# Optimization experiments

Measured on AMD Instinct MI355X. Metric: run time of the kernel, lower is better.

Reference implementation:

```python
import jax, jax.numpy as jnp
import numpy as np

NEG = -1e9


def _siglu(x):
    return x * jax.nn.sigmoid(x)


def setup_inputs() -> dict:
    key = jax.random.key(0)
    ks = jax.random.split(key, 10)
    B, S, M, D = 2, 2048, 64, 1024
    sc = 0.02
    return {
        "tokens": jax.random.normal(ks[0], (B, S, D), jnp.float32),
        "memory": jax.random.normal(ks[1], (B, M, D), jnp.float32),
        "Wq": jax.random.normal(ks[2], (D, D), jnp.float32) * sc,
        "bq": jnp.zeros((D,), jnp.float32),
        "Wk": jax.random.normal(ks[3], (D, D), jnp.float32) * sc,
        "bk": jnp.zeros((D,), jnp.float32),
        "Wv": jax.random.normal(ks[4], (D, D), jnp.float32) * sc,
        "bv": jnp.zeros((D,), jnp.float32),
        "Wo": jax.random.normal(ks[5], (D, D), jnp.float32) * sc,
        "bo": jnp.zeros((D,), jnp.float32),
        "pool_q": jax.random.normal(ks[6], (M, D), jnp.float32),
        "cell_W": jax.random.normal(ks[7], (2 * D, 2 * D), jnp.float32) * sc,
        "cell_b": jnp.zeros((2 * D,), jnp.float32),
    }


def reference(tokens, memory, Wq, bq, Wk, bk, Wv, bv, Wo, bo, pool_q, cell_W, cell_b):
    B, S, D = tokens.shape
    M = memory.shape[1]
    H = 16
    hd = D // H
    T = M + S

    x = jnp.concatenate([memory, tokens], axis=1)  # (B, T, D)

    # combined causal mask: memory rows/cols fully visible, token block causal
    tok_mask = jnp.triu(jnp.full((S, S), NEG, jnp.float32), k=1)
    mask = jnp.zeros((T, T), jnp.float32).at[M:, M:].set(tok_mask)  # (T, T)

    def heads(w, b):
        return (x @ w.T + b).reshape(B, T, H, hd).transpose(0, 2, 1, 3)

    q = heads(Wq, bq)  # (B, H, T, hd)
    k = heads(Wk, bk)
    v = heads(Wv, bv)

    scores = jnp.einsum("bhqd,bhkd->bhqk", q, k) * (hd ** -0.5) + mask
    attn = jax.nn.softmax(scores, axis=-1)
    ctx = jnp.einsum("bhqk,bhkd->bhqd", attn, v)
    ctx = ctx.transpose(0, 2, 1, 3).reshape(B, T, D)
    attn_out = ctx @ Wo.T + bo

    x = x + attn_out  # residual
    mem_out = x[:, :M]  # (B, M, D)
    tok_out = x[:, M:]  # (B, S, D)

    # attention pooling: one learnable query per memory slot
    pscores = jnp.einsum("md,bsd->bms", pool_q, tok_out) * (D ** -0.5)
    pweights = jax.nn.softmax(pscores, axis=-1)
    summary = jnp.einsum("bms,bsd->bmd", pweights, tok_out)  # (B, M, D)

    # MinimalRNNCell (siglu-gated) applied per memory slot
    combined = jnp.concatenate([mem_out, summary], axis=-1)  # (B, M, 2D)
    update = combined @ cell_W.T + cell_b
    gate, cand = jnp.split(update, 2, axis=-1)
    gate = jax.nn.sigmoid(gate)
    new_memory = mem_out * gate + (1.0 - gate) * _siglu(cand)

    return tok_out, new_memory
```

## Files before the change

### kernel.cpp

```cpp
#include <hip/hip_runtime.h>
#include <hip/hip_bf16.h>

#define B_  2
#define S_  2048
#define M_  64
#define D_  1024
#define T_  2112
#define H_  16
#define HD_ 64
#define BT_ (B_*T_)
#define NEGBIG (-1e9f)
#define LOG2E 1.44269504f

typedef float f32x4  __attribute__((ext_vector_type(4)));
typedef short short8 __attribute__((ext_vector_type(8)));
typedef __bf16 bf16x8 __attribute__((ext_vector_type(8)));

static __device__ __forceinline__ unsigned short bf16_of(float f) {
  __hip_bfloat16 h = __float2bfloat16(f);
  return __builtin_bit_cast(unsigned short, h);
}

static __device__ __forceinline__ f32x4 mfma_bf16(short8 a, short8 b, f32x4 c) {
  return __builtin_amdgcn_mfma_f32_16x16x32_bf16(
      __builtin_bit_cast(bf16x8, a), __builtin_bit_cast(bf16x8, b), c, 0, 0, 0);
}

static __device__ __forceinline__ void gload16(const void* g, void* lds) {
  __builtin_amdgcn_global_load_lds(
      (const __attribute__((address_space(1))) unsigned int*)g,
      (__attribute__((address_space(3))) unsigned int*)lds, 16, 0, 0);
}


__global__ void k_build_x(const float* __restrict__ tokens,
                          const float* __restrict__ memory,
                          unsigned short* __restrict__ xb) {
  for (int i = blockIdx.x * blockDim.x + threadIdx.x; i < BT_ * D_;
       i += gridDim.x * blockDim.x) {
    int b = i / (T_ * D_);
    int rem = i - b * (T_ * D_);
    int t = rem / D_;
    int d = rem - t * D_;
    float v = (t < M_) ? memory[((size_t)b * M_ + t) * D_ + d]
                       : tokens[((size_t)b * S_ + (t - M_)) * D_ + d];
    xb[i] = bf16_of(v);
  }
}

__global__ void k_cast_all(const float* __restrict__ Wq, const float* __restrict__ Wk,
                           const float* __restrict__ Wv, const float* __restrict__ Wo,
                           const float* __restrict__ cW, const float* __restrict__ pq,
                           unsigned short* __restrict__ Wqkvb, unsigned short* __restrict__ Wob,
                           unsigned short* __restrict__ cWb, unsigned short* __restrict__ pqb) {
  const int NW = D_ * D_;
  const int NC = 4 * D_ * D_;
  const int NP = M_ * D_;
  const int total = 4 * NW + NC + NP;
  for (int i = blockIdx.x * blockDim.x + threadIdx.x; i < total;
       i += gridDim.x * blockDim.x) {
    if (i < 3 * NW) {
      int which = i >> 20, j = i & (NW - 1);
      const float* s = (which == 0) ? Wq : (which == 1) ? Wk : Wv;
      Wqkvb[i] = bf16_of(s[j]);
    } else if (i < 4 * NW) {
      int j = i - 3 * NW;
      Wob[j] = bf16_of(Wo[j]);
    } else if (i < 4 * NW + NC) {
      int j = i - 4 * NW;
      cWb[j] = bf16_of(cW[j]);
    } else {
      int j = i - 4 * NW - NC;
      pqb[j] = bf16_of(pq[j] * 0.03125f * LOG2E);
    }
  }
}

__device__ __forceinline__ void gemm128_core(const unsigned short* __restrict__ A,
                                             const unsigned short* __restrict__ BT,
                                             int K, int m0, int n0,
                                             f32x4 acc[4][4]) {
  __shared__ __align__(16) unsigned short As[128][32];
  __shared__ __align__(16) unsigned short Bs[128][32];
  const int tid = threadIdx.x;
  const int w = tid >> 6, l = tid & 63;
  const int wr = w >> 1, wc = w & 1;
  const int srow = l >> 2;
  const int scol = (l & 3) * 8;
  f32x4 z; z[0] = z[1] = z[2] = z[3] = 0.f;
#pragma unroll
  for (int i = 0; i < 4; i++)
#pragma unroll
    for (int j = 0; j < 4; j++) acc[i][j] = z;

  for (int k0 = 0; k0 < K; k0 += 32) {
    __syncthreads();
#pragma unroll
    for (int c = 0; c < 2; c++) {
      int rbase = w * 32 + c * 16;
      gload16(&A[(size_t)(m0 + rbase + srow) * K + k0 + scol], &As[rbase][0]);
      gload16(&BT[(size_t)(n0 + rbase + srow) * K + k0 + scol], &Bs[rbase][0]);
    }
    __syncthreads();
    short8 a[4], b[4];
#pragma unroll
    for (int i = 0; i < 4; i++)
      a[i] = *(const short8*)&As[wr * 64 + i * 16 + (l & 15)][(l >> 4) * 8];
#pragma unroll
    for (int j = 0; j < 4; j++)
      b[j] = *(const short8*)&Bs[wc * 64 + j * 16 + (l & 15)][(l >> 4) * 8];
#pragma unroll
    for (int i = 0; i < 4; i++)
#pragma unroll
      for (int j = 0; j < 4; j++)
        acc[i][j] = mfma_bf16(a[i], b[j], acc[i][j]);
  }
}

__device__ __forceinline__ void gemm_core(const unsigned short* __restrict__ A,
                                          const unsigned short* __restrict__ BT,
                                          int ldk, int Klen, int m0, int n0,
                                          f32x4 acc[4]) {
  __shared__ __align__(16) unsigned short As[64][40];
  __shared__ __align__(16) unsigned short Bs[64][40];
  const int tid = threadIdx.x;
  const int w = tid >> 6, l = tid & 63;
  const int sr = tid >> 2, sc = (tid & 3) * 8;
  f32x4 z; z[0] = z[1] = z[2] = z[3] = 0.f;
  acc[0] = acc[1] = acc[2] = acc[3] = z;
  for (int k0 = 0; k0 < Klen; k0 += 32) {
    __syncthreads();
    *(short8*)&As[sr][sc] = *(const short8*)&A[(size_t)(m0 + sr) * ldk + k0 + sc];
    *(short8*)&Bs[sr][sc] = *(const short8*)&BT[(size_t)(n0 + sr) * ldk + k0 + sc];
    __syncthreads();
    short8 a = *(const short8*)&As[w * 16 + (l & 15)][(l >> 4) * 8];
#pragma unroll
    for (int n = 0; n < 4; n++) {
      short8 b = *(const short8*)&Bs[n * 16 + (l & 15)][(l >> 4) * 8];
      acc[n] = mfma_bf16(a, b, acc[n]);
    }
  }
}

__global__ __launch_bounds__(256) void k_qkv(
    const unsigned short* __restrict__ xb, const unsigned short* __restrict__ Wqkvb,
    const float* __restrict__ bq, const float* __restrict__ bk,
    const float* __restrict__ bv, unsigned short* __restrict__ qg,
    unsigned short* __restrict__ kg, unsigned short* __restrict__ vTg) {
  const int which = blockIdx.x >> 3;
  const unsigned short* W = Wqkvb + (size_t)which * D_ * D_;
  const float* bias = (which == 0) ? bq : ((which == 1) ? bk : bv);
  f32x4 acc[4][4];
  const int m0 = blockIdx.y * 128, n0 = (blockIdx.x & 7) * 128;
  gemm128_core(xb, W, D_, m0, n0, acc);
  const int tid = threadIdx.x, w = tid >> 6, l = tid & 63;
  const int wr = w >> 1, wc = w & 1;
#pragma unroll
  for (int i = 0; i < 4; i++) {
#pragma unroll
    for (int j = 0; j < 4; j++) {
#pragma unroll
      for (int r = 0; r < 4; r++) {
        int m = m0 + wr * 64 + i * 16 + (l >> 4) * 4 + r;
        int c = n0 + wc * 64 + j * 16 + (l & 15);
        int b = m / T_, t = m - b * T_;
        int h = c >> 6, dh = c & 63;
        int bh = b * H_ + h;
        float v = acc[i][j][r] + bias[c];
        if (which == 0)
          qg[((size_t)bh * T_ + t) * HD_ + dh] = bf16_of(v * 0.125f * LOG2E);
        else if (which == 1)
          kg[((size_t)bh * T_ + t) * HD_ + dh] = bf16_of(v);
        else
          vTg[((size_t)bh * HD_ + dh) * T_ + t] = bf16_of(v);
      }
    }
  }
}

__global__ __launch_bounds__(256) void k_attn(
    const unsigned short* __restrict__ qg, const unsigned short* __restrict__ kg,
    const unsigned short* __restrict__ vTg, unsigned short* __restrict__ ctx) {
  const int id = blockIdx.x;
  const int xcd = id & 7;
  const int rem = id >> 3;
  const int g = rem / 33, qtr = rem - g * 33;
  const int qt = 32 - qtr;
  const int bh = g * 8 + xcd;
  const int tid = threadIdx.x, w = tid >> 6, l = tid & 63;
  const int lr = l & 15, lg = l >> 4;
  __shared__ __align__(16) unsigned short Ks[2][64][64];
  __shared__ __align__(16) unsigned short Vs[2][64][64];
  __shared__ __align__(16) unsigned short Ps[4][16][72];

  const unsigned short* qb = qg + (size_t)bh * T_ * HD_;
  const unsigned short* kb = kg + (size_t)bh * T_ * HD_;
  const unsigned short* vb = vTg + (size_t)bh * HD_ * T_;

  short8 aq[2];
  const int qrow = qt * 64 + w * 16 + lr;
#pragma unroll
  for (int st = 0; st < 2; st++)
    aq[st] = *(const short8*)&qb[(size_t)qrow * HD_ + st * 32 + lg * 8];

  f32x4 zz; zz[0] = zz[1] = zz[2] = zz[3] = 0.f;
  f32x4 o[4];
  o[0] = o[1] = o[2] = o[3] = zz;
  float mrun[4], lrun[4];
#pragma unroll
  for (int r = 0; r < 4; r++) { mrun[r] = -1e30f; lrun[r] = 0.f; }

  const int nkt = (qt == 0) ? 33 : qt + 1;

  auto stage = [&](int buf, int kb2) {
#pragma unroll
    for (int i = 0; i < 2; i++) {
      int rr = w * 16 + i * 8 + (l >> 3);
      int swz = ((l & 7) ^ (rr & 7)) * 8;
      gload16(&kb[(size_t)(kb2 + rr) * HD_ + swz], &Ks[buf][w * 16 + i * 8][0]);
      gload16(&vb[(size_t)rr * T_ + kb2 + swz], &Vs[buf][w * 16 + i * 8][0]);
    }
  };

  stage(0, 0);
  __syncthreads();
  int cur = 0;

  for (int j = 0; j < nkt; j++) {
    const int kbase = j * 64;
    if (j + 1 < nkt) stage(cur ^ 1, kbase + 64);

    short8 bkf[2][4];
#pragma unroll
    for (int n = 0; n < 4; n++) {
      int row = n * 16 + lr;
      int sw = lr & 7;
#pragma unroll
      for (int st = 0; st < 2; st++)
        bkf[st][n] = *(const short8*)&Ks[cur][row][((st * 4 + lg) ^ sw) * 8];
    }
    f32x4 s[4];
    s[0] = s[1] = s[2] = s[3] = zz;
#pragma unroll
    for (int st = 0; st < 2; st++)
#pragma unroll
      for (int n = 0; n < 4; n++)
        s[n] = mfma_bf16(aq[st], bkf[st][n], s[n]);

    if (qt > 0 && j == qt) {
#pragma unroll
      for (int n = 0; n < 4; n++)
#pragma unroll
        for (int r = 0; r < 4; r++) {
          int t1l = w * 16 + lg * 4 + r;
          int t2l = n * 16 + lr;
          if (t2l > t1l) s[n][r] = NEGBIG;
        }
    }
    float pm[4];
#pragma unroll
    for (int r = 0; r < 4; r++) {
      pm[r] = fmaxf(fmaxf(s[0][r], s[1][r]), fmaxf(s[2][r], s[3][r]));
#pragma unroll
      for (int mk = 1; mk < 16; mk <<= 1) pm[r] = fmaxf(pm[r], __shfl_xor(pm[r], mk));
    }
    bool need = false;
#pragma unroll
    for (int r = 0; r < 4; r++) need = need || (pm[r] > mrun[r] + 8.f);
    if (__any(need)) {
#pragma unroll
      for (int r = 0; r < 4; r++) {
        float mn = fmaxf(mrun[r], pm[r]);
        float fac = exp2f(mrun[r] - mn);
        mrun[r] = mn;
        lrun[r] *= fac;
#pragma unroll
        for (int n = 0; n < 4; n++) o[n][r] *= fac;
      }
    }
#pragma unroll
    for (int n = 0; n < 4; n++)
#pragma unroll
      for (int r = 0; r < 4; r++) {
        float p = exp2f(s[n][r] - mrun[r]);
        lrun[r] += p;
        Ps[w][lg * 4 + r][n * 16 + lr] = bf16_of(p);
      }

    short8 bvf[2][4];
#pragma unroll
    for (int n = 0; n < 4; n++) {
      int row = n * 16 + lr;
      int sw = lr & 7;
#pragma unroll
      for (int st = 0; st < 2; st++)
        bvf[st][n] = *(const short8*)&Vs[cur][row][((st * 4 + lg) ^ sw) * 8];
    }
    short8 ap[2];
#pragma unroll
    for (int st = 0; st < 2; st++)
      ap[st] = *(const short8*)&Ps[w][lr][st * 32 + lg * 8];
#pragma unroll
    for (int st = 0; st < 2; st++)
#pragma unroll
      for (int n = 0; n < 4; n++)
        o[n] = mfma_bf16(ap[st], bvf[st][n], o[n]);

    __syncthreads();
    cur ^= 1;
  }
#pragma unroll
  for (int r = 0; r < 4; r++)
#pragma unroll
    for (int mk = 1; mk < 16; mk <<= 1) lrun[r] += __shfl_xor(lrun[r], mk);

  const int b = bh >> 4, h = bh & 15;
#pragma unroll
  for (int n = 0; n < 4; n++)
#pragma unroll
    for (int r = 0; r < 4; r++) {
      int tq = qt * 64 + w * 16 + lg * 4 + r;
      float val = o[n][r] / lrun[r];
      ctx[((size_t)(b * T_ + tq)) * D_ + h * HD_ + n * 16 + lr] = bf16_of(val);
    }
}

__global__ __launch_bounds__(256) void k_out(
    const unsigned short* __restrict__ ctxb, const unsigned short* __restrict__ Wob,
    const float* __restrict__ bo, const float* __restrict__ tokens,
    const float* __restrict__ memory, float* __restrict__ out_tok,
    unsigned short* __restrict__ tokb, unsigned short* __restrict__ tokTb,
    float* __restrict__ memout, unsigned short* __restrict__ comb) {
  f32x4 acc[4][4];
  const int m0 = blockIdx.y * 128, n0 = blockIdx.x * 128;
  gemm128_core(ctxb, Wob, D_, m0, n0, acc);
  const int tid = threadIdx.x, w = tid >> 6, l = tid & 63;
  const int wr = w >> 1, wc = w & 1;
#pragma unroll
  for (int i = 0; i < 4; i++) {
#pragma unroll
    for (int j = 0; j < 4; j++) {
#pragma unroll
      for (int r = 0; r < 4; r++) {
        int m = m0 + wr * 64 + i * 16 + (l >> 4) * 4 + r;
        int c = n0 + wc * 64 + j * 16 + (l & 15);
        int b = m / T_, t = m - b * T_;
        float xo = (t < M_) ? memory[((size_t)b * M_ + t) * D_ + c]
                            : tokens[((size_t)b * S_ + (t - M_)) * D_ + c];
        float val = acc[i][j][r] + bo[c] + xo;
        if (t < M_) {
          memout[((size_t)b * M_ + t) * D_ + c] = val;
          comb[((size_t)b * M_ + t) * (2 * D_) + c] = bf16_of(val);
        } else {
          size_t ti = (size_t)b * S_ + (t - M_);
          out_tok[ti * D_ + c] = val;
          tokb[ti * D_ + c] = bf16_of(val);
          tokTb[((size_t)b * D_ + c) * S_ + (t - M_)] = bf16_of(val);
        }
      }
    }
  }
}

__global__ __launch_bounds__(256) void k_pscore_part(
    const unsigned short* __restrict__ pqb, const unsigned short* __restrict__ tokb,
    float* __restrict__ pscp) {
  const int stile = blockIdx.x, ks = blockIdx.y, b = blockIdx.z;
  f32x4 acc[4];
  gemm_core(pqb + ks * 256, tokb + (size_t)b * S_ * D_ + ks * 256, D_, 256,
            0, stile * 64, acc);
  const int tid = threadIdx.x, w = tid >> 6, l = tid & 63;
  float* dst = pscp + ((size_t)(ks * B_ + b) * M_) * S_;
#pragma unroll
  for (int n = 0; n < 4; n++) {
#pragma unroll
    for (int r = 0; r < 4; r++) {
      int m = w * 16 + (l >> 4) * 4 + r;
      int s = stile * 64 + n * 16 + (l & 15);
      dst[(size_t)m * S_ + s] = acc[n][r];
    }
  }
}

__global__ __launch_bounds__(256) void k_psoftmax(const float* __restrict__ pscp,
                                                  unsigned short* __restrict__ pw) {
  const int row = blockIdx.x;
  const int b = row >> 6, m = row & 63;
  const int tid = threadIdx.x;
  float v[8];
  float mx = -1e30f;
#pragma unroll
  for (int i = 0; i < 8; i++) {
    int s = tid + i * 256;
    float acc = 0.f;
#pragma unroll
    for (int ks = 0; ks < 4; ks++)
      acc += pscp[((size_t)(ks * B_ + b) * M_ + m) * S_ + s];
    v[i] = acc;
    mx = fmaxf(mx, acc);
  }
#pragma unroll
  for (int off = 1; off < 64; off <<= 1) mx = fmaxf(mx, __shfl_xor(mx, off));
  __shared__ float rm[4], rs[4];
  if ((tid & 63) == 0) rm[tid >> 6] = mx;
  __syncthreads();
  mx = fmaxf(fmaxf(rm[0], rm[1]), fmaxf(rm[2], rm[3]));
  float sum = 0.f;
#pragma unroll
  for (int i = 0; i < 8; i++) {
    v[i] = exp2f(v[i] - mx);
    sum += v[i];
  }
#pragma unroll
  for (int off = 1; off < 64; off <<= 1) sum += __shfl_xor(sum, off);
  if ((tid & 63) == 0) rs[tid >> 6] = sum;
  __syncthreads();
  float inv = 1.f / (rs[0] + rs[1] + rs[2] + rs[3]);
#pragma unroll
  for (int i = 0; i < 8; i++)
    pw[(size_t)row * S_ + tid + i * 256] = bf16_of(v[i] * inv);
}

__global__ __launch_bounds__(256) void k_summary_part(
    const unsigned short* __restrict__ pw, const unsigned short* __restrict__ tokTb,
    float* __restrict__ sump) {
  const int nt = blockIdx.x, ks = blockIdx.y, b = blockIdx.z;
  f32x4 acc[4];
  gemm_core(pw + (size_t)b * M_ * S_ + ks * 256,
            tokTb + (size_t)b * D_ * S_ + ks * 256, S_, 256, 0, nt * 64, acc);
  const int tid = threadIdx.x, w = tid >> 6, l = tid & 63;
  float* dst = sump + ((size_t)(ks * B_ + b) * M_) * D_;
#pragma unroll
  for (int n = 0; n < 4; n++) {
#pragma unroll
    for (int r = 0; r < 4; r++) {
      int m = w * 16 + (l >> 4) * 4 + r;
      int c = nt * 64 + n * 16 + (l & 15);
      dst[(size_t)m * D_ + c] = acc[n][r];
    }
  }
}

__global__ void k_sumcomb(const float* __restrict__ sump,
                          unsigned short* __restrict__ comb) {
  int i = blockIdx.x * blockDim.x + threadIdx.x;
  if (i >= B_ * M_ * D_) return;
  int bm = i >> 10, c = i & 1023;
  int b = bm >> 6, m = bm & 63;
  float acc = 0.f;
#pragma unroll
  for (int ks = 0; ks < 8; ks++)
    acc += sump[((size_t)(ks * B_ + b) * M_ + m) * D_ + c];
  comb[((size_t)b * M_ + m) * (2 * D_) + D_ + c] = bf16_of(acc);
}

__global__ __launch_bounds__(256) void k_cell_part(
    const unsigned short* __restrict__ comb, const unsigned short* __restrict__ cWb,
    float* __restrict__ cellp) {
  const int nt = blockIdx.x, mt = blockIdx.y, ks = blockIdx.z;
  f32x4 acc[4];
  gemm_core(comb + ks * 512, cWb + ks * 512, 2 * D_, 512, mt * 64, nt * 64, acc);
  const int tid = threadIdx.x, w = tid >> 6, l = tid & 63;
#pragma unroll
  for (int n = 0; n < 4; n++) {
#pragma unroll
    for (int r = 0; r < 4; r++) {
      int m = mt * 64 + w * 16 + (l >> 4) * 4 + r;
      int c = nt * 64 + n * 16 + (l & 15);
      cellp[((size_t)ks * (B_ * M_) + m) * (2 * D_) + c] = acc[n][r];
    }
  }
}

__global__ void k_newmem(const float* __restrict__ cellp,
                         const float* __restrict__ cb,
                         const float* __restrict__ memout,
                         float* __restrict__ out2) {
  int i = blockIdx.x * blockDim.x + threadIdx.x;
  if (i >= B_ * M_ * D_) return;
  int r = i >> 10, d = i & 1023;
  float gsum = cb[d], csum = cb[D_ + d];
#pragma unroll
  for (int ks = 0; ks < 4; ks++) {
    gsum += cellp[((size_t)ks * (B_ * M_) + r) * (2 * D_) + d];
    csum += cellp[((size_t)ks * (B_ * M_) + r) * (2 * D_) + D_ + d];
  }
  float sg = 1.f / (1.f + __expf(-gsum));
  float sc = 1.f / (1.f + __expf(-csum));
  out2[i] = memout[i] * sg + (1.f - sg) * (csum * sc);
}

extern "C" void kernel_launch(void* const* d_in, const int* in_sizes, int n_in,
                              void* d_out, int out_size, void* d_ws, size_t ws_size,
                              hipStream_t stream) {
  const float* tokens = (const float*)d_in[0];
  const float* memory = (const float*)d_in[1];
  const float* Wq = (const float*)d_in[2];
  const float* bq = (const float*)d_in[3];
  const float* Wk = (const float*)d_in[4];
  const float* bk = (const float*)d_in[5];
  const float* Wv = (const float*)d_in[6];
  const float* bv = (const float*)d_in[7];
  const float* Wo = (const float*)d_in[8];
  const float* bo = (const float*)d_in[9];
  const float* pool_q = (const float*)d_in[10];
  const float* cell_W = (const float*)d_in[11];
  const float* cell_b = (const float*)d_in[12];

  size_t off = 0;
  auto alloc = [&](size_t bytes) -> void* {
    void* p = (char*)d_ws + off;
    off += (bytes + 255) & ~(size_t)255;
    return p;
  };
  unsigned short* xb    = (unsigned short*)alloc((size_t)BT_ * D_ * 2);
  unsigned short* Wqkvb = (unsigned short*)alloc((size_t)3 * D_ * D_ * 2);
  unsigned short* Wob   = (unsigned short*)alloc((size_t)D_ * D_ * 2);
  unsigned short* cWb   = (unsigned short*)alloc((size_t)(2 * D_) * (2 * D_) * 2);
  unsigned short* pqb   = (unsigned short*)alloc((size_t)M_ * D_ * 2);
  unsigned short* qg    = (unsigned short*)alloc((size_t)B_ * H_ * T_ * HD_ * 2);
  unsigned short* kg    = (unsigned short*)alloc((size_t)B_ * H_ * T_ * HD_ * 2);
  unsigned short* vTg   = (unsigned short*)alloc((size_t)B_ * H_ * HD_ * T_ * 2);
  unsigned short* ctxb  = (unsigned short*)alloc((size_t)BT_ * D_ * 2);
  unsigned short* tokb  = (unsigned short*)alloc((size_t)B_ * S_ * D_ * 2);
  unsigned short* tokTb = (unsigned short*)alloc((size_t)B_ * D_ * S_ * 2);
  float*          memout= (float*)alloc((size_t)B_ * M_ * D_ * 4);
  unsigned short* comb  = (unsigned short*)alloc((size_t)B_ * M_ * 2 * D_ * 2);
  unsigned short* pwt   = (unsigned short*)alloc((size_t)B_ * M_ * S_ * 2);
  float*          pscp  = (float*)alloc((size_t)4 * B_ * M_ * S_ * 4);
  float*          sump  = (float*)alloc((size_t)8 * B_ * M_ * D_ * 4);
  float*          cellp = (float*)alloc((size_t)4 * B_ * M_ * 2 * D_ * 4);

  float* out_tok = (float*)d_out;
  float* out_mem = out_tok + (size_t)B_ * S_ * D_;

  k_build_x<<<2048, 256, 0, stream>>>(tokens, memory, xb);
  k_cast_all<<<4096, 256, 0, stream>>>(Wq, Wk, Wv, Wo, cell_W, pool_q,
                                       Wqkvb, Wob, cWb, pqb);

  k_qkv<<<dim3(24, 33), 256, 0, stream>>>(xb, Wqkvb, bq, bk, bv, qg, kg, vTg);
  k_attn<<<1056, 256, 0, stream>>>(qg, kg, vTg, ctxb);
  k_out<<<dim3(8, 33), 256, 0, stream>>>(ctxb, Wob, bo, tokens, memory, out_tok,
                                         tokb, tokTb, memout, comb);
  k_pscore_part<<<dim3(32, 4, 2), 256, 0, stream>>>(pqb, tokb, pscp);
  k_psoftmax<<<B_ * M_, 256, 0, stream>>>(pscp, pwt);
  k_summary_part<<<dim3(16, 8, 2), 256, 0, stream>>>(pwt, tokTb, sump);
  k_sumcomb<<<512, 256, 0, stream>>>(sump, comb);
  k_cell_part<<<dim3(32, 2, 4), 256, 0, stream>>>(comb, cWb, cellp);
  k_newmem<<<512, 256, 0, stream>>>(cellp, cell_b, memout, out_mem);
}
```

Baseline: 240.5 us.

## Transpose QK^T MFMA so each lane owns a query row in attention softmax

Swaps the MFMA operands for the score product so every lane holds one query row across four key columns. The row max and row sum then need two cross-lane shuffles instead of four per register. The P tile is written to LDS with one packed 4-element store per lane instead of scalar stores. The rescale factor and the final 1/l are broadcast back to the output layout with shuffles, and the division becomes a multiply. The change also adds s_setprio around the MFMA blocks and reorders the work so the longest-running query tiles start first.

```diff
diff --git a/kernel.cpp b/kernel.cpp
--- a/kernel.cpp
+++ b/kernel.cpp
@@ -14,6 +14,7 @@
 
 typedef float f32x4  __attribute__((ext_vector_type(4)));
 typedef short short8 __attribute__((ext_vector_type(8)));
+typedef unsigned short u16x4 __attribute__((ext_vector_type(4)));
 typedef __bf16 bf16x8 __attribute__((ext_vector_type(8)));
 
 static __device__ __forceinline__ unsigned short bf16_of(float f) {
@@ -185,7 +186,7 @@
   const int xcd = id & 7;
   const int rem = id >> 3;
   const int g = rem / 33, qtr = rem - g * 33;
-  const int qt = 32 - qtr;
+  const int qt = (qtr == 0) ? 0 : 33 - qtr;
   const int bh = g * 8 + xcd;
   const int tid = threadIdx.x, w = tid >> 6, l = tid & 63;
   const int lr = l & 15, lg = l >> 4;
@@ -206,9 +207,7 @@
   f32x4 zz; zz[0] = zz[1] = zz[2] = zz[3] = 0.f;
   f32x4 o[4];
   o[0] = o[1] = o[2] = o[3] = zz;
-  float mrun[4], lrun[4];
-#pragma unroll
-  for (int r = 0; r < 4; r++) { mrun[r] = -1e30f; lrun[r] = 0.f; }
+  float mrun = -1e30f, lrun = 0.f;
 
   const int nkt = (qt == 0) ? 33 : qt + 1;
 
@@ -241,51 +240,56 @@
     }
     f32x4 s[4];
     s[0] = s[1] = s[2] = s[3] = zz;
+    __builtin_amdgcn_s_setprio(1);
 #pragma unroll
     for (int st = 0; st < 2; st++)
 #pragma unroll
       for (int n = 0; n < 4; n++)
-        s[n] = mfma_bf16(aq[st], bkf[st][n], s[n]);
+        s[n] = mfma_bf16(bkf[st][n], aq[st], s[n]);
+    __builtin_amdgcn_s_setprio(0);
 
     if (qt > 0 && j == qt) {
+      const int tql = w * 16 + lr;
 #pragma unroll
       for (int n = 0; n < 4; n++)
 #pragma unroll
         for (int r = 0; r < 4; r++) {
-          int t1l = w * 16 + lg * 4 + r;
-          int t2l = n * 16 + lr;
-          if (t2l > t1l) s[n][r] = NEGBIG;
+          int tkl = n * 16 + lg * 4 + r;
+          if (tkl > tql) s[n][r] = NEGBIG;
         }
     }
-    float pm[4];
-#pragma unroll
-    for (int r = 0; r < 4; r++) {
-      pm[r] = fmaxf(fmaxf(s[0][r], s[1][r]), fmaxf(s[2][r], s[3][r]));
-#pragma unroll
-      for (int mk = 1; mk < 16; mk <<= 1) pm[r] = fmaxf(pm[r], __shfl_xor(pm[r], mk));
-    }
-    bool need = false;
-#pragma unroll
-    for (int r = 0; r < 4; r++) need = need || (pm[r] > mrun[r] + 8.f);
-    if (__any(need)) {
+    float pm = s[0][0];
+#pragma unroll
+    for (int n = 0; n < 4; n++)
+#pragma unroll
+      for (int r = 0; r < 4; r++) pm = fmaxf(pm, s[n][r]);
+    pm = fmaxf(pm, __shfl_xor(pm, 16));
+    pm = fmaxf(pm, __shfl_xor(pm, 32));
+
+    if (__any(pm > mrun + 8.f)) {
+      float mn = fmaxf(mrun, pm);
+      float fac = exp2f(mrun - mn);
+      mrun = mn;
+      lrun *= fac;
+      float fr[4];
+#pragma unroll
+      for (int r = 0; r < 4; r++) fr[r] = __shfl(fac, lg * 4 + r);
+#pragma unroll
+      for (int n = 0; n < 4; n++)
+#pragma unroll
+        for (int r = 0; r < 4; r++) o[n][r] *= fr[r];
+    }
+#pragma unroll
+    for (int n = 0; n < 4; n++) {
+      u16x4 pk;
 #pragma unroll
       for (int r = 0; r < 4; r++) {
-        float mn = fmaxf(mrun[r], pm[r]);
-        float fac = exp2f(mrun[r] - mn);
-        mrun[r] = mn;
-        lrun[r] *= fac;
-#pragma unroll
-        for (int n = 0; n < 4; n++) o[n][r] *= fac;
+        float p = exp2f(s[n][r] - mrun);
+        lrun += p;
+        pk[r] = bf16_of(p);
       }
-    }
-#pragma unroll
-    for (int n = 0; n < 4; n++)
-#pragma unroll
-      for (int r = 0; r < 4; r++) {
-        float p = exp2f(s[n][r] - mrun[r]);
-        lrun[r] += p;
-        Ps[w][lg * 4 + r][n * 16 + lr] = bf16_of(p);
-      }
+      *(u16x4*)&Ps[w][lr][n * 16 + lg * 4] = pk;
+    }
 
     short8 bvf[2][4];
 #pragma unroll
@@ -300,19 +304,22 @@
 #pragma unroll
     for (int st = 0; st < 2; st++)
       ap[st] = *(const short8*)&Ps[w][lr][st * 32 + lg * 8];
+    __builtin_amdgcn_s_setprio(1);
 #pragma unroll
     for (int st = 0; st < 2; st++)
 #pragma unroll
       for (int n = 0; n < 4; n++)
         o[n] = mfma_bf16(ap[st], bvf[st][n], o[n]);
+    __builtin_amdgcn_s_setprio(0);
 
     __syncthreads();
     cur ^= 1;
   }
-#pragma unroll
-  for (int r = 0; r < 4; r++)
-#pragma unroll
-    for (int mk = 1; mk < 16; mk <<= 1) lrun[r] += __shfl_xor(lrun[r], mk);
+  lrun += __shfl_xor(lrun, 16);
+  lrun += __shfl_xor(lrun, 32);
+  float linv[4];
+#pragma unroll
+  for (int r = 0; r < 4; r++) linv[r] = 1.f / __shfl(lrun, lg * 4 + r);
 
   const int b = bh >> 4, h = bh & 15;
 #pragma unroll
@@ -320,7 +327,7 @@
 #pragma unroll
     for (int r = 0; r < 4; r++) {
       int tq = qt * 64 + w * 16 + lg * 4 + r;
-      float val = o[n][r] / lrun[r];
+      float val = o[n][r] * linv[r];
       ctx[((size_t)(b * T_ + tq)) * D_ + h * HD_ + n * 16 + lr] = bf16_of(val);
     }
 }
```

New measurement: 219.5 us. 8.8% less time.
